# Optimization experiments

Hardware: AMD Instinct MI355X
Metric: run time of the kernel (lower is better)

The kernel has to match this reference:

```python
import math
import jax, jax.numpy as jnp
import numpy as np

L = 5  # local_context_length
H = 8  # heads


def _local_pool(x, L):
    """Causal local-window softmax pooling.
    For each position i, window = positions [i-L+1, i] (zero-padded at front),
    weights = softmax(x_i . x_window / sqrt(D)), pooled_i = sum_j w_ij * x_window_j.
    x: [B, S, D] -> [B, S, D]."""
    B, S, D = x.shape
    xp = jnp.pad(x, ((0, 0), (L - 1, 0), (0, 0)))          # [B, S+L-1, D]
    idx = jnp.arange(S)[:, None] + jnp.arange(L)[None, :]   # [S, L] window gather indices
    win = xp[:, idx, :]                                     # [B, S, L, D]
    scores = jnp.einsum('bsd,bsld->bsl', x, win) / jnp.asarray(math.sqrt(D), x.dtype)
    w = jax.nn.softmax(scores, axis=-1)                     # [B, S, L]
    return jnp.einsum('bsl,bsld->bsd', w, win)              # [B, S, D]


def setup_inputs() -> dict:
    key0 = jax.random.key(0)
    ks = jax.random.split(key0, 10)
    B, S, D = 4, 2048, 512
    scale = 1.0 / math.sqrt(D)
    return {
        'query': jax.random.normal(ks[0], (B, S, D), jnp.float32),
        'key':   jax.random.normal(ks[1], (B, S, D), jnp.float32),
        'value': jax.random.normal(ks[2], (B, S, D), jnp.float32),
        'mask':  jnp.ones((S, S), jnp.int32),  # dead: forward passes mask=None to attention
        'W_fk':  jax.random.normal(ks[3], (D, D), jnp.float32) * scale,
        'b_fk':  jnp.zeros((D,), jnp.float32),
        'W0':    jax.random.normal(ks[4], (D, D), jnp.float32) * scale,
        'b0':    jnp.zeros((D,), jnp.float32),
        'Wout':  jax.random.normal(ks[5], (D, D), jnp.float32) * scale,
        'bout':  jnp.zeros((D,), jnp.float32),
    }


def reference(query, key, value, mask, W_fk, b_fk, W0, b0, Wout, bout):
    B, S, D = query.shape
    dk = D // H

    q = _local_pool(query, L)                                # [B,S,D]
    k = _local_pool(key @ W_fk + b_fk, L)                    # feature_weight_linear then pool
    v = value @ W0 + b0                                      # linears[0]

    def split(x):  # [B,S,D] -> [B,H,S,dk]
        return x.reshape(B, S, H, dk).transpose(0, 2, 1, 3)

    qh, kh, vh = split(q), split(k), split(v)
    scores = jnp.einsum('bhqd,bhkd->bhqk', qh, kh) / jnp.asarray(math.sqrt(dk), q.dtype)
    p = jax.nn.softmax(scores, axis=-1)                      # mask=None, dropout off (eval)
    x = jnp.einsum('bhqk,bhkd->bhqd', p, vh)
    x = x.transpose(0, 2, 1, 3).reshape(B, S, D)
    return x @ Wout + bout                                   # linears[-1]
```

## Files before the change

kernel.cpp:

```cpp
#include <hip/hip_runtime.h>
#include <hip/hip_bf16.h>
#include <math.h>

#define B_  4
#define S_  2048
#define D_  512
#define H_  8
#define DK_ 64
#define BS_ (B_*S_)

using bf16x8 = __attribute__((ext_vector_type(8))) short;
using f32x4  = __attribute__((ext_vector_type(4))) float;
using f32x16 = __attribute__((ext_vector_type(16))) float;

typedef const __attribute__((address_space(1))) unsigned int gu32;
typedef __attribute__((address_space(3))) unsigned int lu32;

static __device__ inline unsigned short f2bf(float a) {
  union { __hip_bfloat16 h; unsigned short u; } x;
  x.h = __float2bfloat16(a); return x.u;
}
static __device__ inline float bf16f(unsigned short u) {
  union { unsigned u32; float f; } x; x.u32 = (unsigned)u << 16; return x.f;
}
static __device__ inline unsigned pk2(float a, float b) {
  unsigned r;
  asm("v_cvt_pk_bf16_f32 %0, %1, %2" : "=v"(r) : "v"(a), "v"(b));
  return r;
}
static __device__ inline float ex2(float a) {
  return __builtin_amdgcn_exp2f(a);
}

template <int SPLIT, int OUTMODE>
__global__ __launch_bounds__(256) void gemm_mfma_kernel(
    const float* __restrict__ A, const float* __restrict__ W,
    const float* __restrict__ bias, void* __restrict__ Cv) {
  const int bn = blockIdx.x;
  const int bm = blockIdx.y;
  const int tid = threadIdx.x;
  const int wv = tid >> 6, lane = tid & 63;
  const int c = lane & 15, g = lane >> 4;

  __shared__ unsigned short As[SPLIT + 1][128][72];
  __shared__ unsigned short Wt[SPLIT + 1][64][72];

  f32x4 acc[2][4];
#pragma unroll
  for (int rt = 0; rt < 2; ++rt)
#pragma unroll
    for (int ds = 0; ds < 4; ++ds) acc[rt][ds] = f32x4{0.f, 0.f, 0.f, 0.f};

  const int arow = tid >> 1, ah = (tid & 1) * 32;
  const int wn = tid & 63, wkg = (tid >> 6) * 16;

  for (int k0 = 0; k0 < D_; k0 += 64) {
    float af[32];
    const float* ag = A + ((size_t)(bm * 128 + arow)) * D_ + k0 + ah;
#pragma unroll
    for (int i = 0; i < 8; ++i) *(float4*)&af[i * 4] = *(const float4*)(ag + i * 4);
    float wf[16];
    const float* wg = W + (size_t)(k0 + wkg) * D_ + bn * 64 + wn;
#pragma unroll
    for (int i = 0; i < 16; ++i) wf[i] = wg[(size_t)i * D_];

    __syncthreads();
#pragma unroll
    for (int grp = 0; grp < 4; ++grp) {
      unsigned h[4], l[4];
#pragma unroll
      for (int p = 0; p < 4; ++p) {
        float f0 = af[grp * 8 + p * 2], f1 = af[grp * 8 + p * 2 + 1];
        h[p] = pk2(f0, f1);
        if constexpr (SPLIT)
          l[p] = pk2(f0 - bf16f((unsigned short)(h[p] & 0xffff)),
                     f1 - bf16f((unsigned short)(h[p] >> 16)));
      }
      uint4 uh; uh.x = h[0]; uh.y = h[1]; uh.z = h[2]; uh.w = h[3];
      *(uint4*)&As[0][arow][ah + grp * 8] = uh;
      if constexpr (SPLIT) {
        uint4 ul; ul.x = l[0]; ul.y = l[1]; ul.z = l[2]; ul.w = l[3];
        *(uint4*)&As[1][arow][ah + grp * 8] = ul;
      }
    }
#pragma unroll
    for (int grp = 0; grp < 2; ++grp) {
      unsigned h[4], l[4];
#pragma unroll
      for (int p = 0; p < 4; ++p) {
        float f0 = wf[grp * 8 + p * 2], f1 = wf[grp * 8 + p * 2 + 1];
        h[p] = pk2(f0, f1);
        if constexpr (SPLIT)
          l[p] = pk2(f0 - bf16f((unsigned short)(h[p] & 0xffff)),
                     f1 - bf16f((unsigned short)(h[p] >> 16)));
      }
      uint4 uh; uh.x = h[0]; uh.y = h[1]; uh.z = h[2]; uh.w = h[3];
      *(uint4*)&Wt[0][wn][wkg + grp * 8] = uh;
      if constexpr (SPLIT) {
        uint4 ul; ul.x = l[0]; ul.y = l[1]; ul.z = l[2]; ul.w = l[3];
        *(uint4*)&Wt[1][wn][wkg + grp * 8] = ul;
      }
    }
    __syncthreads();

#pragma unroll
    for (int ksub = 0; ksub < 2; ++ksub) {
      bf16x8 bh[2], bl[2];
#pragma unroll
      for (int rt = 0; rt < 2; ++rt) {
        bh[rt] = *(const bf16x8*)&As[0][wv * 32 + rt * 16 + c][ksub * 32 + g * 8];
        if constexpr (SPLIT)
          bl[rt] = *(const bf16x8*)&As[1][wv * 32 + rt * 16 + c][ksub * 32 + g * 8];
      }
#pragma unroll
      for (int ds = 0; ds < 4; ++ds) {
        bf16x8 ah_ = *(const bf16x8*)&Wt[0][ds * 16 + c][ksub * 32 + g * 8];
#pragma unroll
        for (int rt = 0; rt < 2; ++rt)
          acc[rt][ds] = __builtin_amdgcn_mfma_f32_16x16x32_bf16(ah_, bh[rt], acc[rt][ds], 0, 0, 0);
        if constexpr (SPLIT) {
          bf16x8 al_ = *(const bf16x8*)&Wt[1][ds * 16 + c][ksub * 32 + g * 8];
#pragma unroll
          for (int rt = 0; rt < 2; ++rt) {
            acc[rt][ds] = __builtin_amdgcn_mfma_f32_16x16x32_bf16(ah_, bl[rt], acc[rt][ds], 0, 0, 0);
            acc[rt][ds] = __builtin_amdgcn_mfma_f32_16x16x32_bf16(al_, bh[rt], acc[rt][ds], 0, 0, 0);
          }
        }
      }
    }
  }

#pragma unroll
  for (int rt = 0; rt < 2; ++rt) {
    const size_t m = (size_t)bm * 128 + wv * 32 + rt * 16 + c;
#pragma unroll
    for (int ds = 0; ds < 4; ++ds) {
      const int n = bn * 64 + ds * 16 + 4 * g;
      float4 bv = *(const float4*)&bias[n];
      float o0 = acc[rt][ds][0] + bv.x, o1 = acc[rt][ds][1] + bv.y;
      float o2 = acc[rt][ds][2] + bv.z, o3 = acc[rt][ds][3] + bv.w;
      if constexpr (OUTMODE == 1) {
        uint2 p; p.x = pk2(o0, o1); p.y = pk2(o2, o3);
        *(uint2*)((unsigned short*)Cv + m * D_ + n) = p;
      } else if constexpr (OUTMODE == 2) {
        const unsigned u01 = pk2(o0, o1), u23 = pk2(o2, o3);
        unsigned short* base =
            (unsigned short*)Cv + ((size_t)(m >> 11) * D_ + n) * (size_t)S_ + (m & 2047);
        base[0]        = (unsigned short)u01;
        base[S_]       = (unsigned short)(u01 >> 16);
        base[2 * S_]   = (unsigned short)u23;
        base[3 * S_]   = (unsigned short)(u23 >> 16);
      } else {
        float4 o; o.x = o0; o.y = o1; o.z = o2; o.w = o3;
        *(float4*)((float*)Cv + m * D_ + n) = o;
      }
    }
  }
}

__global__ __launch_bounds__(256) void local_pool_kernel(
    const float* __restrict__ x, unsigned short* __restrict__ out,
    float oscale) {
  const int gtid = blockIdx.x * 256 + threadIdx.x;
  const int wave = gtid >> 6;
  const int lane = gtid & 63;
  if (wave >= BS_) return;
  const int b = wave / S_, s = wave % S_;
  const float* xrow = x + ((size_t)b * S_ + s) * D_;
  const int d0 = lane * 8;
  float xi[8];
  *(float4*)&xi[0] = *(const float4*)&xrow[d0];
  *(float4*)&xi[4] = *(const float4*)&xrow[d0 + 4];
  float win[5][8];
  float sc[5];
#pragma unroll
  for (int j = 0; j < 5; ++j) {
    int src = s - 4 + j;
    float part = 0.f;
    if (src >= 0) {
      const float* wr = x + ((size_t)b * S_ + src) * D_;
      *(float4*)&win[j][0] = *(const float4*)&wr[d0];
      *(float4*)&win[j][4] = *(const float4*)&wr[d0 + 4];
#pragma unroll
      for (int t = 0; t < 8; ++t) part += xi[t] * win[j][t];
    } else {
#pragma unroll
      for (int t = 0; t < 8; ++t) win[j][t] = 0.f;
    }
    sc[j] = part;
  }
#pragma unroll
  for (int off = 1; off < 64; off <<= 1) {
#pragma unroll
    for (int j = 0; j < 5; ++j) sc[j] += __shfl_xor(sc[j], off, 64);
  }
  const float scale = 0.04419417382415922f;
  float m = sc[0] * scale;
#pragma unroll
  for (int j = 1; j < 5; ++j) m = fmaxf(m, sc[j] * scale);
  float w[5], lsum = 0.f;
#pragma unroll
  for (int j = 0; j < 5; ++j) { w[j] = expf(sc[j] * scale - m); lsum += w[j]; }
  const float inv = oscale / lsum;
  float o[8] = {};
#pragma unroll
  for (int j = 0; j < 5; ++j)
#pragma unroll
    for (int t = 0; t < 8; ++t) o[t] += w[j] * win[j][t];
  unsigned short* orow = out + ((size_t)b * S_ + s) * D_;
  uint4 pk;
  pk.x = pk2(o[0] * inv, o[1] * inv);
  pk.y = pk2(o[2] * inv, o[3] * inv);
  pk.z = pk2(o[4] * inv, o[5] * inv);
  pk.w = pk2(o[6] * inv, o[7] * inv);
  *(uint4*)&orow[d0] = pk;
}

__global__ __launch_bounds__(256, 2) void attn_mfma32_kernel(
    const unsigned short* __restrict__ q, const unsigned short* __restrict__ k,
    const unsigned short* __restrict__ vt, float* __restrict__ x) {
  const int bid = (blockIdx.x & 7) * 128 + (blockIdx.x >> 3);
  const int qb = bid & 31;
  const int h  = (bid >> 5) & 7;
  const int b  = bid >> 8;
  const int tid = threadIdx.x;
  const int w = tid >> 6, l = tid & 63;
  const int ql = l & 31, hi = l >> 5;
  const int wq = w & 1, wh = w >> 1;

  __shared__ __align__(16) unsigned short L[2][2][2][4096];

  bf16x8 Qf[4];
  {
    const unsigned short* qg =
        q + ((size_t)b * S_ + qb * 64 + wq * 32 + ql) * D_ + h * 64 + hi * 8;
#pragma unroll
    for (int f = 0; f < 4; ++f) Qf[f] = *(const bf16x8*)(qg + f * 16);
  }

  f32x16 accO[2] = {};
  float m = -INFINITY, lsum = 0.f;

  const int lr8 = l >> 3, lc = l & 7;
  const unsigned short* kg =
      k + ((size_t)b * S_ + wh * 1024 + wq * 32 + lr8) * D_ + h * 64 + ((lc ^ lr8) << 3);
  const unsigned short* vg =
      vt + ((size_t)b * D_ + h * 64 + wq * 32 + lr8) * (size_t)S_ + wh * 1024 + ((lc ^ lr8) << 3);

  auto ISSUE = [&](int t, int bf) {
    const unsigned short* kp = kg + (size_t)t * 64 * D_;
    const unsigned short* vp = vg + t * 64;
    char* dk = (char*)&L[bf][0][wh][0] + wq * 4096;
    char* dv = (char*)&L[bf][1][wh][0] + wq * 4096;
#pragma unroll
    for (int j = 0; j < 4; ++j) {
      __builtin_amdgcn_global_load_lds((gu32*)(kp + (size_t)j * 8 * D_),
                                       (lu32*)(dk + j * 1024), 16, 0, 0);
      __builtin_amdgcn_global_load_lds((gu32*)(vp + (size_t)j * 8 * S_),
                                       (lu32*)(dv + j * 1024), 16, 0, 0);
    }
  };

  ISSUE(0, 0);
  asm volatile("s_waitcnt vmcnt(0)" ::: "memory");
  __builtin_amdgcn_s_barrier();
  __builtin_amdgcn_sched_barrier(0);

  int cur = 0;
  for (int kt = 0; kt < 16; ++kt) {
    if (kt + 1 < 16) ISSUE(kt + 1, cur ^ 1);
    __builtin_amdgcn_sched_barrier(0);
    const char* KsB = (const char*)&L[cur][0][wh][0];
    const char* VtB = (const char*)&L[cur][1][wh][0];

    f32x16 sA = {}, sB = {};
    __builtin_amdgcn_s_setprio(1);
#pragma unroll
    for (int f = 0; f < 4; ++f) {
      bf16x8 a0 = *(const bf16x8*)(KsB + ((ql * 128 + f * 32 + hi * 16) ^ ((ql & 7) << 4)));
      bf16x8 a1 = *(const bf16x8*)(KsB + (((ql + 32) * 128 + f * 32 + hi * 16) ^ ((ql & 7) << 4)));
      sA = __builtin_amdgcn_mfma_f32_32x32x16_bf16(a0, Qf[f], sA, 0, 0, 0);
      sB = __builtin_amdgcn_mfma_f32_32x32x16_bf16(a1, Qf[f], sB, 0, 0, 0);
    }
    __builtin_amdgcn_s_setprio(0);

    float mx[8];
#pragma unroll
    for (int r = 0; r < 8; ++r)
      mx[r] = fmaxf(fmaxf(sA[r], sA[r + 8]), fmaxf(sB[r], sB[r + 8]));
    mx[0] = fmaxf(mx[0], mx[4]); mx[1] = fmaxf(mx[1], mx[5]);
    mx[2] = fmaxf(mx[2], mx[6]); mx[3] = fmaxf(mx[3], mx[7]);
    mx[0] = fmaxf(fmaxf(mx[0], mx[1]), fmaxf(mx[2], mx[3]));
    const float mt = fmaxf(mx[0], __shfl_xor(mx[0], 32, 64));
    if (!__all(mt <= m + 10.0f)) {
      const float mn = fmaxf(m, mt);
      const float corr = ex2(m - mn);
      m = mn;
      lsum *= corr;
#pragma unroll
      for (int dt = 0; dt < 2; ++dt)
#pragma unroll
        for (int r = 0; r < 16; ++r) accO[dt][r] *= corr;
    }

    unsigned WA[8], WB[8];
    float s0 = 0.f, s1 = 0.f, s2 = 0.f, s3 = 0.f;
#pragma unroll
    for (int t = 0; t < 4; ++t) {
      float a0 = ex2(sA[4 * t + 0] - m), a1 = ex2(sA[4 * t + 1] - m);
      float a2 = ex2(sA[4 * t + 2] - m), a3 = ex2(sA[4 * t + 3] - m);
      WA[2 * t] = pk2(a0, a1); WA[2 * t + 1] = pk2(a2, a3);
      s0 += a0 + a1; s1 += a2 + a3;
      float b0 = ex2(sB[4 * t + 0] - m), b1 = ex2(sB[4 * t + 1] - m);
      float b2 = ex2(sB[4 * t + 2] - m), b3 = ex2(sB[4 * t + 3] - m);
      WB[2 * t] = pk2(b0, b1); WB[2 * t + 1] = pk2(b2, b3);
      s2 += b0 + b1; s3 += b2 + b3;
    }
    lsum += (s0 + s1) + (s2 + s3);

#pragma unroll
    for (int kc = 0; kc < 4; ++kc) {
      unsigned w0 = (kc < 2) ? WA[(kc & 1) * 4 + 0] : WB[(kc & 1) * 4 + 0];
      unsigned w1 = (kc < 2) ? WA[(kc & 1) * 4 + 1] : WB[(kc & 1) * 4 + 1];
      unsigned w2 = (kc < 2) ? WA[(kc & 1) * 4 + 2] : WB[(kc & 1) * 4 + 2];
      unsigned w3 = (kc < 2) ? WA[(kc & 1) * 4 + 3] : WB[(kc & 1) * 4 + 3];
      asm volatile("v_permlane32_swap_b32 %0, %1" : "+v"(w0), "+v"(w2));
      asm volatile("v_permlane32_swap_b32 %0, %1" : "+v"(w1), "+v"(w3));
      union { unsigned u[4]; bf16x8 v8; } pb;
      pb.u[0] = w0; pb.u[1] = w1; pb.u[2] = w2; pb.u[3] = w3;
      __builtin_amdgcn_s_setprio(1);
#pragma unroll
      for (int dt = 0; dt < 2; ++dt) {
        const int vrow = dt * 32 + ql;
        bf16x8 va = *(const bf16x8*)(VtB + ((vrow * 128 + kc * 32 + hi * 16) ^ ((ql & 7) << 4)));
        accO[dt] = __builtin_amdgcn_mfma_f32_32x32x16_bf16(va, pb.v8, accO[dt], 0, 0, 0);
      }
      __builtin_amdgcn_s_setprio(0);
    }

    asm volatile("s_waitcnt vmcnt(0)" ::: "memory");
    __builtin_amdgcn_s_barrier();
    __builtin_amdgcn_sched_barrier(0);
    cur ^= 1;
  }

  float lw = lsum + __shfl_xor(lsum, 32, 64);
  __syncthreads();
  float* cb = (float*)L + (size_t)wq * 2176 + (size_t)l * 34;
  if (wh == 1) {
#pragma unroll
    for (int dt = 0; dt < 2; ++dt)
#pragma unroll
      for (int r = 0; r < 16; ++r) cb[dt * 16 + r] = accO[dt][r];
    cb[32] = m; cb[33] = lw;
  }
  __syncthreads();
  if (wh == 0) {
    const float m1 = cb[32], l1 = cb[33];
    const float mn = fmaxf(m, m1);
    const float a0 = ex2(m - mn), a1 = ex2(m1 - mn);
    const float inv = 1.f / (lw * a0 + l1 * a1);
    float* xrow = x + ((size_t)b * S_ + qb * 64 + wq * 32 + ql) * D_ + h * 64;
#pragma unroll
    for (int dt = 0; dt < 2; ++dt)
#pragma unroll
      for (int g0 = 0; g0 < 4; ++g0) {
        float4 o;
        o.x = (accO[dt][4 * g0 + 0] * a0 + cb[dt * 16 + 4 * g0 + 0] * a1) * inv;
        o.y = (accO[dt][4 * g0 + 1] * a0 + cb[dt * 16 + 4 * g0 + 1] * a1) * inv;
        o.z = (accO[dt][4 * g0 + 2] * a0 + cb[dt * 16 + 4 * g0 + 2] * a1) * inv;
        o.w = (accO[dt][4 * g0 + 3] * a0 + cb[dt * 16 + 4 * g0 + 3] * a1) * inv;
        *(float4*)&xrow[dt * 32 + hi * 4 + g0 * 8] = o;
      }
  }
}

extern "C" void kernel_launch(void* const* d_in, const int* in_sizes, int n_in,
                              void* d_out, int out_size, void* d_ws, size_t ws_size,
                              hipStream_t stream) {
  const float* query = (const float*)d_in[0];
  const float* key   = (const float*)d_in[1];
  const float* value = (const float*)d_in[2];
  const float* W_fk = (const float*)d_in[4];
  const float* b_fk = (const float*)d_in[5];
  const float* W0   = (const float*)d_in[6];
  const float* b0   = (const float*)d_in[7];
  const float* Wout = (const float*)d_in[8];
  const float* bout = (const float*)d_in[9];
  float* out = (float*)d_out;

  char* ws = (char*)d_ws;
  float* kfk_f32   = (float*)ws;
  float* x_f32     = (float*)(ws + (16u << 20));
  unsigned short* k_bf16 = (unsigned short*)(ws + (32u << 20));
  unsigned short* vT_bf16 = (unsigned short*)(ws + (40u << 20));
  unsigned short* q_bf16 = (unsigned short*)ws;

  dim3 mgrid(D_ / 64, BS_ / 128);
  dim3 pgrid(BS_ * 64 / 256);
  const float qscale = 0.125f * 1.4426950408889634f;

  gemm_mfma_kernel<1, 0><<<mgrid, 256, 0, stream>>>(key, W_fk, b_fk, kfk_f32);
  local_pool_kernel<<<pgrid, 256, 0, stream>>>(kfk_f32, k_bf16, 1.0f);
  gemm_mfma_kernel<0, 2><<<mgrid, 256, 0, stream>>>(value, W0, b0, vT_bf16);
  local_pool_kernel<<<pgrid, 256, 0, stream>>>(query, q_bf16, qscale);
  attn_mfma32_kernel<<<dim3(B_ * H_ * (S_ / 64)), 256, 0, stream>>>(q_bf16, k_bf16, vT_bf16, x_f32);
  gemm_mfma_kernel<1, 0><<<mgrid, 256, 0, stream>>>(x_f32, Wout, bout, out);
}
```

Before: 171.5 us.

## Pre-split weights into bf16 planes, prefetch GEMM tiles, emit attention output as bf16 hi/lo

A new prep kernel transposes each weight matrix and splits it into bf16 hi/lo planes once per call. The GEMMs then load those planes with contiguous vector reads instead of strided scalar fp32 reads plus in-kernel conversion. The GEMM main loop now prefetches the next K tile into registers while the current one is computed. The attention kernel writes its output as bf16 hi/lo planes, so the final GEMM reads packed data without converting it. This adds one launch and extra workspace traffic for the weight planes, and raises register pressure from the prefetch.

```diff
diff --git a/kernel.cpp b/kernel.cpp
--- a/kernel.cpp
+++ b/kernel.cpp
@@ -16,10 +16,6 @@
 typedef const __attribute__((address_space(1))) unsigned int gu32;
 typedef __attribute__((address_space(3))) unsigned int lu32;
 
-static __device__ inline unsigned short f2bf(float a) {
-  union { __hip_bfloat16 h; unsigned short u; } x;
-  x.h = __float2bfloat16(a); return x.u;
-}
 static __device__ inline float bf16f(unsigned short u) {
   union { unsigned u32; float f; } x; x.u32 = (unsigned)u << 16; return x.f;
 }
@@ -32,9 +28,60 @@
   return __builtin_amdgcn_exp2f(a);
 }
 
-template <int SPLIT, int OUTMODE>
-__global__ __launch_bounds__(256) void gemm_mfma_kernel(
-    const float* __restrict__ A, const float* __restrict__ W,
+__global__ __launch_bounds__(256) void wprep_kernel(
+    const float* __restrict__ Wfk, const float* __restrict__ W0,
+    const float* __restrict__ Wout,
+    unsigned short* __restrict__ t0h, unsigned short* __restrict__ t0l,
+    unsigned short* __restrict__ t1h,
+    unsigned short* __restrict__ t2h, unsigned short* __restrict__ t2l) {
+  const int bid = blockIdx.x;
+  const int mi = bid >> 6, t = bid & 63;
+  const float* W = (mi == 0) ? Wfk : (mi == 1) ? W0 : Wout;
+  unsigned short* th = (mi == 0) ? t0h : (mi == 1) ? t1h : t2h;
+  unsigned short* tl = (mi == 0) ? t0l : (mi == 1) ? nullptr : t2l;
+  const int kt = t >> 3, nt = t & 7;
+  const int tid = threadIdx.x;
+
+  __shared__ float Ts[64][68];
+  {
+    const int r = tid >> 2, c = (tid & 3) * 16;
+    const float* src = W + (size_t)(kt * 64 + r) * D_ + nt * 64 + c;
+#pragma unroll
+    for (int i = 0; i < 4; ++i)
+      *(float4*)&Ts[r][c + i * 4] = *(const float4*)(src + i * 4);
+  }
+  __syncthreads();
+  {
+    const int n = tid >> 2, kc = (tid & 3) * 16;
+    float v[16];
+#pragma unroll
+    for (int i = 0; i < 16; ++i) v[i] = Ts[kc + i][n];
+    unsigned h[8], l[8];
+#pragma unroll
+    for (int p = 0; p < 8; ++p) {
+      h[p] = pk2(v[2 * p], v[2 * p + 1]);
+      if (tl)
+        l[p] = pk2(v[2 * p] - bf16f((unsigned short)(h[p] & 0xffff)),
+                   v[2 * p + 1] - bf16f((unsigned short)(h[p] >> 16)));
+    }
+    unsigned short* dh = th + (size_t)(nt * 64 + n) * D_ + kt * 64 + kc;
+    uint4 u0; u0.x = h[0]; u0.y = h[1]; u0.z = h[2]; u0.w = h[3];
+    uint4 u1; u1.x = h[4]; u1.y = h[5]; u1.z = h[6]; u1.w = h[7];
+    *(uint4*)dh = u0; *(uint4*)(dh + 8) = u1;
+    if (tl) {
+      unsigned short* dl = tl + (size_t)(nt * 64 + n) * D_ + kt * 64 + kc;
+      uint4 w0; w0.x = l[0]; w0.y = l[1]; w0.z = l[2]; w0.w = l[3];
+      uint4 w1; w1.x = l[4]; w1.y = l[5]; w1.z = l[6]; w1.w = l[7];
+      *(uint4*)dl = w0; *(uint4*)(dl + 8) = w1;
+    }
+  }
+}
+
+template <int SPLIT, int APLANES, int OUTMODE>
+__global__ __launch_bounds__(256) void gemm_v3_kernel(
+    const float* __restrict__ A,
+    const unsigned short* __restrict__ Aph, const unsigned short* __restrict__ Apl,
+    const unsigned short* __restrict__ Wth, const unsigned short* __restrict__ Wtl,
     const float* __restrict__ bias, void* __restrict__ Cv) {
   const int bn = blockIdx.x;
   const int bm = blockIdx.y;
@@ -51,57 +98,74 @@
 #pragma unroll
     for (int ds = 0; ds < 4; ++ds) acc[rt][ds] = f32x4{0.f, 0.f, 0.f, 0.f};
 
-  const int arow = tid >> 1, ah = (tid & 1) * 32;
+  const int arow = tid >> 1, ahh = (tid & 1) * 32;
   const int wn = tid & 63, wkg = (tid >> 6) * 16;
 
+  float afr[32];
+  uint4 ahr[4], alr[4];
+  uint4 whr[2], wlr[2];
+
+  auto LOADT = [&](int k0) {
+    if constexpr (!APLANES) {
+      const float* ag = A + (size_t)(bm * 128 + arow) * D_ + k0 + ahh;
+#pragma unroll
+      for (int i = 0; i < 8; ++i) *(float4*)&afr[i * 4] = *(const float4*)(ag + i * 4);
+    } else {
+      const unsigned short* agh = Aph + (size_t)(bm * 128 + arow) * D_ + k0 + ahh;
+#pragma unroll
+      for (int i = 0; i < 4; ++i) ahr[i] = *(const uint4*)(agh + i * 8);
+      const unsigned short* agl = Apl + (size_t)(bm * 128 + arow) * D_ + k0 + ahh;
+#pragma unroll
+      for (int i = 0; i < 4; ++i) alr[i] = *(const uint4*)(agl + i * 8);
+    }
+    const unsigned short* wgh = Wth + (size_t)(bn * 64 + wn) * D_ + k0 + wkg;
+    whr[0] = *(const uint4*)wgh; whr[1] = *(const uint4*)(wgh + 8);
+    if constexpr (SPLIT) {
+      const unsigned short* wgl = Wtl + (size_t)(bn * 64 + wn) * D_ + k0 + wkg;
+      wlr[0] = *(const uint4*)wgl; wlr[1] = *(const uint4*)(wgl + 8);
+    }
+  };
+  auto STORET = [&]() {
+    if constexpr (!APLANES) {
+#pragma unroll
+      for (int grp = 0; grp < 4; ++grp) {
+        unsigned h[4], l[4];
+#pragma unroll
+        for (int p = 0; p < 4; ++p) {
+          float f0 = afr[grp * 8 + p * 2], f1 = afr[grp * 8 + p * 2 + 1];
+          h[p] = pk2(f0, f1);
+          if constexpr (SPLIT)
+            l[p] = pk2(f0 - bf16f((unsigned short)(h[p] & 0xffff)),
+                       f1 - bf16f((unsigned short)(h[p] >> 16)));
+        }
+        uint4 uh; uh.x = h[0]; uh.y = h[1]; uh.z = h[2]; uh.w = h[3];
+        *(uint4*)&As[0][arow][ahh + grp * 8] = uh;
+        if constexpr (SPLIT) {
+          uint4 ul; ul.x = l[0]; ul.y = l[1]; ul.z = l[2]; ul.w = l[3];
+          *(uint4*)&As[1][arow][ahh + grp * 8] = ul;
+        }
+      }
+    } else {
+#pragma unroll
+      for (int i = 0; i < 4; ++i) {
+        *(uint4*)&As[0][arow][ahh + i * 8] = ahr[i];
+        *(uint4*)&As[1][arow][ahh + i * 8] = alr[i];
+      }
+    }
+    *(uint4*)&Wt[0][wn][wkg] = whr[0];
+    *(uint4*)&Wt[0][wn][wkg + 8] = whr[1];
+    if constexpr (SPLIT) {
+      *(uint4*)&Wt[1][wn][wkg] = wlr[0];
+      *(uint4*)&Wt[1][wn][wkg + 8] = wlr[1];
+    }
+  };
+
+  LOADT(0);
   for (int k0 = 0; k0 < D_; k0 += 64) {
-    float af[32];
-    const float* ag = A + ((size_t)(bm * 128 + arow)) * D_ + k0 + ah;
-#pragma unroll
-    for (int i = 0; i < 8; ++i) *(float4*)&af[i * 4] = *(const float4*)(ag + i * 4);
-    float wf[16];
-    const float* wg = W + (size_t)(k0 + wkg) * D_ + bn * 64 + wn;
-#pragma unroll
-    for (int i = 0; i < 16; ++i) wf[i] = wg[(size_t)i * D_];
-
     __syncthreads();
-#pragma unroll
-    for (int grp = 0; grp < 4; ++grp) {
-      unsigned h[4], l[4];
-#pragma unroll
-      for (int p = 0; p < 4; ++p) {
-        float f0 = af[grp * 8 + p * 2], f1 = af[grp * 8 + p * 2 + 1];
-        h[p] = pk2(f0, f1);
-        if constexpr (SPLIT)
-          l[p] = pk2(f0 - bf16f((unsigned short)(h[p] & 0xffff)),
-                     f1 - bf16f((unsigned short)(h[p] >> 16)));
-      }
-      uint4 uh; uh.x = h[0]; uh.y = h[1]; uh.z = h[2]; uh.w = h[3];
-      *(uint4*)&As[0][arow][ah + grp * 8] = uh;
-      if constexpr (SPLIT) {
-        uint4 ul; ul.x = l[0]; ul.y = l[1]; ul.z = l[2]; ul.w = l[3];
-        *(uint4*)&As[1][arow][ah + grp * 8] = ul;
-      }
-    }
-#pragma unroll
-    for (int grp = 0; grp < 2; ++grp) {
-      unsigned h[4], l[4];
-#pragma unroll
-      for (int p = 0; p < 4; ++p) {
-        float f0 = wf[grp * 8 + p * 2], f1 = wf[grp * 8 + p * 2 + 1];
-        h[p] = pk2(f0, f1);
-        if constexpr (SPLIT)
-          l[p] = pk2(f0 - bf16f((unsigned short)(h[p] & 0xffff)),
-                     f1 - bf16f((unsigned short)(h[p] >> 16)));
-      }
-      uint4 uh; uh.x = h[0]; uh.y = h[1]; uh.z = h[2]; uh.w = h[3];
-      *(uint4*)&Wt[0][wn][wkg + grp * 8] = uh;
-      if constexpr (SPLIT) {
-        uint4 ul; ul.x = l[0]; ul.y = l[1]; ul.z = l[2]; ul.w = l[3];
-        *(uint4*)&Wt[1][wn][wkg + grp * 8] = ul;
-      }
-    }
+    STORET();
     __syncthreads();
+    if (k0 + 64 < D_) LOADT(k0 + 64);
 
 #pragma unroll
     for (int ksub = 0; ksub < 2; ++ksub) {
@@ -139,17 +203,14 @@
       float4 bv = *(const float4*)&bias[n];
       float o0 = acc[rt][ds][0] + bv.x, o1 = acc[rt][ds][1] + bv.y;
       float o2 = acc[rt][ds][2] + bv.z, o3 = acc[rt][ds][3] + bv.w;
-      if constexpr (OUTMODE == 1) {
-        uint2 p; p.x = pk2(o0, o1); p.y = pk2(o2, o3);
-        *(uint2*)((unsigned short*)Cv + m * D_ + n) = p;
-      } else if constexpr (OUTMODE == 2) {
+      if constexpr (OUTMODE == 2) {
         const unsigned u01 = pk2(o0, o1), u23 = pk2(o2, o3);
         unsigned short* base =
             (unsigned short*)Cv + ((size_t)(m >> 11) * D_ + n) * (size_t)S_ + (m & 2047);
-        base[0]        = (unsigned short)u01;
-        base[S_]       = (unsigned short)(u01 >> 16);
-        base[2 * S_]   = (unsigned short)u23;
-        base[3 * S_]   = (unsigned short)(u23 >> 16);
+        base[0]      = (unsigned short)u01;
+        base[S_]     = (unsigned short)(u01 >> 16);
+        base[2 * S_] = (unsigned short)u23;
+        base[3 * S_] = (unsigned short)(u23 >> 16);
       } else {
         float4 o; o.x = o0; o.y = o1; o.z = o2; o.w = o3;
         *(float4*)((float*)Cv + m * D_ + n) = o;
@@ -218,7 +279,8 @@
 
 __global__ __launch_bounds__(256, 2) void attn_mfma32_kernel(
     const unsigned short* __restrict__ q, const unsigned short* __restrict__ k,
-    const unsigned short* __restrict__ vt, float* __restrict__ x) {
+    const unsigned short* __restrict__ vt,
+    unsigned short* __restrict__ xh, unsigned short* __restrict__ xl) {
   const int bid = (blockIdx.x & 7) * 128 + (blockIdx.x >> 3);
   const int qb = bid & 31;
   const int h  = (bid >> 5) & 7;
@@ -360,17 +422,27 @@
     const float mn = fmaxf(m, m1);
     const float a0 = ex2(m - mn), a1 = ex2(m1 - mn);
     const float inv = 1.f / (lw * a0 + l1 * a1);
-    float* xrow = x + ((size_t)b * S_ + qb * 64 + wq * 32 + ql) * D_ + h * 64;
+    const size_t rowoff = ((size_t)b * S_ + qb * 64 + wq * 32 + ql) * D_ + h * 64;
+    unsigned short* xhr = xh + rowoff;
+    unsigned short* xlr = xl + rowoff;
 #pragma unroll
     for (int dt = 0; dt < 2; ++dt)
 #pragma unroll
       for (int g0 = 0; g0 < 4; ++g0) {
-        float4 o;
-        o.x = (accO[dt][4 * g0 + 0] * a0 + cb[dt * 16 + 4 * g0 + 0] * a1) * inv;
-        o.y = (accO[dt][4 * g0 + 1] * a0 + cb[dt * 16 + 4 * g0 + 1] * a1) * inv;
-        o.z = (accO[dt][4 * g0 + 2] * a0 + cb[dt * 16 + 4 * g0 + 2] * a1) * inv;
-        o.w = (accO[dt][4 * g0 + 3] * a0 + cb[dt * 16 + 4 * g0 + 3] * a1) * inv;
-        *(float4*)&xrow[dt * 32 + hi * 4 + g0 * 8] = o;
+        float ox = (accO[dt][4 * g0 + 0] * a0 + cb[dt * 16 + 4 * g0 + 0] * a1) * inv;
+        float oy = (accO[dt][4 * g0 + 1] * a0 + cb[dt * 16 + 4 * g0 + 1] * a1) * inv;
+        float oz = (accO[dt][4 * g0 + 2] * a0 + cb[dt * 16 + 4 * g0 + 2] * a1) * inv;
+        float ow = (accO[dt][4 * g0 + 3] * a0 + cb[dt * 16 + 4 * g0 + 3] * a1) * inv;
+        unsigned h01 = pk2(ox, oy), h23 = pk2(oz, ow);
+        unsigned l01 = pk2(ox - bf16f((unsigned short)(h01 & 0xffff)),
+                           oy - bf16f((unsigned short)(h01 >> 16)));
+        unsigned l23 = pk2(oz - bf16f((unsigned short)(h23 & 0xffff)),
+                           ow - bf16f((unsigned short)(h23 >> 16)));
+        const int off = dt * 32 + hi * 4 + g0 * 8;
+        uint2 uh_; uh_.x = h01; uh_.y = h23;
+        uint2 ul_; ul_.x = l01; ul_.y = l23;
+        *(uint2*)&xhr[off] = uh_;
+        *(uint2*)&xlr[off] = ul_;
       }
   }
 }
@@ -390,20 +462,32 @@
   float* out = (float*)d_out;
 
   char* ws = (char*)d_ws;
-  float* kfk_f32   = (float*)ws;
-  float* x_f32     = (float*)(ws + (16u << 20));
-  unsigned short* k_bf16 = (unsigned short*)(ws + (32u << 20));
-  unsigned short* vT_bf16 = (unsigned short*)(ws + (40u << 20));
-  unsigned short* q_bf16 = (unsigned short*)ws;
+  unsigned short* wfk_h  = (unsigned short*)(ws);
+  unsigned short* wfk_l  = (unsigned short*)(ws + (512u << 10));
+  unsigned short* w0_h   = (unsigned short*)(ws + (1024u << 10));
+  unsigned short* wout_h = (unsigned short*)(ws + (1536u << 10));
+  unsigned short* wout_l = (unsigned short*)(ws + (2048u << 10));
+  float*          kfk_f32 = (float*)(ws + (3u << 20));
+  unsigned short* q_bf16  = (unsigned short*)(ws + (3u << 20));
+  unsigned short* vT_bf16 = (unsigned short*)(ws + (11u << 20));
+  unsigned short* xh      = (unsigned short*)(ws + (19u << 20));
+  unsigned short* xl      = (unsigned short*)(ws + (27u << 20));
+  unsigned short* k_bf16  = (unsigned short*)(ws + (35u << 20));
 
   dim3 mgrid(D_ / 64, BS_ / 128);
   dim3 pgrid(BS_ * 64 / 256);
   const float qscale = 0.125f * 1.4426950408889634f;
 
-  gemm_mfma_kernel<1, 0><<<mgrid, 256, 0, stream>>>(key, W_fk, b_fk, kfk_f32);
+  wprep_kernel<<<192, 256, 0, stream>>>(W_fk, W0, Wout,
+                                        wfk_h, wfk_l, w0_h, wout_h, wout_l);
+  gemm_v3_kernel<1, 0, 0><<<mgrid, 256, 0, stream>>>(
+      key, nullptr, nullptr, wfk_h, wfk_l, b_fk, kfk_f32);
   local_pool_kernel<<<pgrid, 256, 0, stream>>>(kfk_f32, k_bf16, 1.0f);
-  gemm_mfma_kernel<0, 2><<<mgrid, 256, 0, stream>>>(value, W0, b0, vT_bf16);
+  gemm_v3_kernel<0, 0, 2><<<mgrid, 256, 0, stream>>>(
+      value, nullptr, nullptr, w0_h, nullptr, b0, vT_bf16);
   local_pool_kernel<<<pgrid, 256, 0, stream>>>(query, q_bf16, qscale);
-  attn_mfma32_kernel<<<dim3(B_ * H_ * (S_ / 64)), 256, 0, stream>>>(q_bf16, k_bf16, vT_bf16, x_f32);
-  gemm_mfma_kernel<1, 0><<<mgrid, 256, 0, stream>>>(x_f32, Wout, bout, out);
-}
+  attn_mfma32_kernel<<<dim3(B_ * H_ * (S_ / 64)), 256, 0, stream>>>(
+      q_bf16, k_bf16, vT_bf16, xh, xl);
+  gemm_v3_kernel<1, 1, 0><<<mgrid, 256, 0, stream>>>(
+      nullptr, xh, xl, wout_h, wout_l, bout, out);
+}
```

Result: slower. 223.7 us (+30.4%).

## Single-buffer V tile and split K/V prefetch to fit three attention blocks per CU

Applied to the files above, without the earlier changes.

Shared memory in the attention kernel is split into a double-buffered K tile and a single-buffered V tile, shrinking the footprint so three blocks can be resident per CU, and launch bounds are raised to match. The K prefetch for the next tile now starts after the QK^T MFMAs. The V load for the next tile is issued after the PV stage, with extra barriers and partial vmcnt waits to order the buffers. The aim is more latency hiding through occupancy. In exchange there are more barriers per tile, less overlap of V loads with compute, and a tighter register budget that could cause spills.

```diff
diff --git a/kernel.cpp b/kernel.cpp
--- a/kernel.cpp
+++ b/kernel.cpp
@@ -16,10 +16,6 @@
 typedef const __attribute__((address_space(1))) unsigned int gu32;
 typedef __attribute__((address_space(3))) unsigned int lu32;
 
-static __device__ inline unsigned short f2bf(float a) {
-  union { __hip_bfloat16 h; unsigned short u; } x;
-  x.h = __float2bfloat16(a); return x.u;
-}
 static __device__ inline float bf16f(unsigned short u) {
   union { unsigned u32; float f; } x; x.u32 = (unsigned)u << 16; return x.f;
 }
@@ -146,10 +142,10 @@
         const unsigned u01 = pk2(o0, o1), u23 = pk2(o2, o3);
         unsigned short* base =
             (unsigned short*)Cv + ((size_t)(m >> 11) * D_ + n) * (size_t)S_ + (m & 2047);
-        base[0]        = (unsigned short)u01;
-        base[S_]       = (unsigned short)(u01 >> 16);
-        base[2 * S_]   = (unsigned short)u23;
-        base[3 * S_]   = (unsigned short)(u23 >> 16);
+        base[0]      = (unsigned short)u01;
+        base[S_]     = (unsigned short)(u01 >> 16);
+        base[2 * S_] = (unsigned short)u23;
+        base[3 * S_] = (unsigned short)(u23 >> 16);
       } else {
         float4 o; o.x = o0; o.y = o1; o.z = o2; o.w = o3;
         *(float4*)((float*)Cv + m * D_ + n) = o;
@@ -216,7 +212,7 @@
   *(uint4*)&orow[d0] = pk;
 }
 
-__global__ __launch_bounds__(256, 2) void attn_mfma32_kernel(
+__global__ __launch_bounds__(256, 3) void attn_mfma32_kernel(
     const unsigned short* __restrict__ q, const unsigned short* __restrict__ k,
     const unsigned short* __restrict__ vt, float* __restrict__ x) {
   const int bid = (blockIdx.x & 7) * 128 + (blockIdx.x >> 3);
@@ -228,7 +224,8 @@
   const int ql = l & 31, hi = l >> 5;
   const int wq = w & 1, wh = w >> 1;
 
-  __shared__ __align__(16) unsigned short L[2][2][2][4096];
+  __shared__ __align__(16) unsigned short Kb[2][2][4096];
+  __shared__ __align__(16) unsigned short Vb[2][4096];
 
   bf16x8 Qf[4];
   {
@@ -247,31 +244,33 @@
   const unsigned short* vg =
       vt + ((size_t)b * D_ + h * 64 + wq * 32 + lr8) * (size_t)S_ + wh * 1024 + ((lc ^ lr8) << 3);
 
-  auto ISSUE = [&](int t, int bf) {
+  auto ISSUE_K = [&](int t, int bf) {
     const unsigned short* kp = kg + (size_t)t * 64 * D_;
-    const unsigned short* vp = vg + t * 64;
-    char* dk = (char*)&L[bf][0][wh][0] + wq * 4096;
-    char* dv = (char*)&L[bf][1][wh][0] + wq * 4096;
-#pragma unroll
-    for (int j = 0; j < 4; ++j) {
+    char* dk = (char*)&Kb[bf][wh][0] + wq * 4096;
+#pragma unroll
+    for (int j = 0; j < 4; ++j)
       __builtin_amdgcn_global_load_lds((gu32*)(kp + (size_t)j * 8 * D_),
                                        (lu32*)(dk + j * 1024), 16, 0, 0);
+  };
+  auto ISSUE_V = [&](int t) {
+    const unsigned short* vp = vg + t * 64;
+    char* dv = (char*)&Vb[wh][0] + wq * 4096;
+#pragma unroll
+    for (int j = 0; j < 4; ++j)
       __builtin_amdgcn_global_load_lds((gu32*)(vp + (size_t)j * 8 * S_),
                                        (lu32*)(dv + j * 1024), 16, 0, 0);
-    }
   };
 
-  ISSUE(0, 0);
+  ISSUE_K(0, 0);
+  ISSUE_V(0);
   asm volatile("s_waitcnt vmcnt(0)" ::: "memory");
   __builtin_amdgcn_s_barrier();
   __builtin_amdgcn_sched_barrier(0);
 
   int cur = 0;
   for (int kt = 0; kt < 16; ++kt) {
-    if (kt + 1 < 16) ISSUE(kt + 1, cur ^ 1);
-    __builtin_amdgcn_sched_barrier(0);
-    const char* KsB = (const char*)&L[cur][0][wh][0];
-    const char* VtB = (const char*)&L[cur][1][wh][0];
+    const char* KsB = (const char*)&Kb[cur][wh][0];
+    const char* VtB = (const char*)&Vb[wh][0];
 
     f32x16 sA = {}, sB = {};
     __builtin_amdgcn_s_setprio(1);
@@ -283,6 +282,9 @@
       sB = __builtin_amdgcn_mfma_f32_32x32x16_bf16(a1, Qf[f], sB, 0, 0, 0);
     }
     __builtin_amdgcn_s_setprio(0);
+
+    if (kt + 1 < 16) ISSUE_K(kt + 1, cur ^ 1);
+    __builtin_amdgcn_sched_barrier(0);
 
     float mx[8];
 #pragma unroll
@@ -318,6 +320,11 @@
     }
     lsum += (s0 + s1) + (s2 + s3);
 
+    if (kt + 1 < 16) asm volatile("s_waitcnt vmcnt(4)" ::: "memory");
+    else             asm volatile("s_waitcnt vmcnt(0)" ::: "memory");
+    __builtin_amdgcn_s_barrier();
+    __builtin_amdgcn_sched_barrier(0);
+
 #pragma unroll
     for (int kc = 0; kc < 4; ++kc) {
       unsigned w0 = (kc < 2) ? WA[(kc & 1) * 4 + 0] : WB[(kc & 1) * 4 + 0];
@@ -338,15 +345,20 @@
       __builtin_amdgcn_s_setprio(0);
     }
 
-    asm volatile("s_waitcnt vmcnt(0)" ::: "memory");
     __builtin_amdgcn_s_barrier();
     __builtin_amdgcn_sched_barrier(0);
+    if (kt + 1 < 16) {
+      ISSUE_V(kt + 1);
+      asm volatile("s_waitcnt vmcnt(4)" ::: "memory");
+      __builtin_amdgcn_s_barrier();
+      __builtin_amdgcn_sched_barrier(0);
+    }
     cur ^= 1;
   }
 
   float lw = lsum + __shfl_xor(lsum, 32, 64);
   __syncthreads();
-  float* cb = (float*)L + (size_t)wq * 2176 + (size_t)l * 34;
+  float* cb = (float*)Kb + (size_t)wq * 2176 + (size_t)l * 34;
   if (wh == 1) {
 #pragma unroll
     for (int dt = 0; dt < 2; ++dt)
```

Result: no change. 172.1 us (+0.3%).
